# Kernel optimization log

Hardware: AMD Instinct MI355X
Metric: run time of the kernel (lower is better)

The kernel has to match this reference:

```python
import jax, jax.numpy as jnp
import numpy as np

NUM_POSES = 4096
NUM_PATCHES = 262144
NUM_OBS = 2097152


def setup_inputs() -> dict:
    key = jax.random.key(0)
    ks = jax.random.split(key, 7)
    poses = jax.random.normal(ks[0], (NUM_POSES, 7), dtype=jnp.float32)
    patch_coords = jax.random.normal(ks[1], (NUM_PATCHES, 2), dtype=jnp.float32)
    elevation_angle = jax.random.normal(ks[2], (NUM_PATCHES, 1), dtype=jnp.float32)
    poses_idx = jax.random.randint(ks[3], (NUM_OBS,), 0, NUM_POSES)
    patch_idx = jax.random.randint(ks[4], (NUM_OBS,), 0, NUM_PATCHES)
    target_coords = jax.random.normal(ks[5], (NUM_OBS, 3), dtype=jnp.float32)
    weights = jax.random.uniform(ks[6], (NUM_OBS, 1), dtype=jnp.float32)
    return {
        "poses": poses,
        "patch_coords": patch_coords,
        "elevation_angle": elevation_angle,
        "poses_idx": poses_idx,
        "patch_idx": patch_idx,
        "target_coords": target_coords,
        "weights": weights,
    }


def _se3_apply(pose7, pts):
    # pose7: [M,7] = (tx,ty,tz,qx,qy,qz,qw); pts: [M,3]
    # Equivalent to transform_matrix(pose) @ [pts; 1] (rotation by unit quaternion + translation)
    t = pose7[:, :3]
    q = pose7[:, 3:]
    q = q / jnp.linalg.norm(q, axis=-1, keepdims=True)  # pp.SE3 keeps unit quats
    qv, qw = q[:, :3], q[:, 3:4]
    uv = jnp.cross(qv, pts)                     # [M,3]
    rotated = pts + 2.0 * (qw * uv + jnp.cross(qv, uv))
    return rotated + t


def _cart2polar(xyz):
    # (x,y,z) -> (range, azimuth, elevation)
    x, y, z = xyz[:, 0], xyz[:, 1], xyz[:, 2]
    rho = jnp.sqrt(x * x + y * y)
    r = jnp.sqrt(rho * rho + z * z)
    az = jnp.arctan2(y, x)
    el = jnp.arctan2(z, rho)
    return jnp.stack([r, az, el], axis=1)


def reference(poses, patch_coords, elevation_angle, poses_idx, patch_idx, target_coords, weights):
    p = poses[poses_idx]                                            # [M,7] gather
    pts = jnp.concatenate(
        [patch_coords[patch_idx], elevation_angle[patch_idx]], axis=1
    )                                                               # [M,3] gather+cat
    proj = _cart2polar(_se3_apply(p, pts))                          # [M,3]
    residual = (proj - target_coords) * weights                     # [M,3]
    return residual
```

## Files before the change

kernel.cpp:

```cpp
#include <hip/hip_runtime.h>
#include <hip/hip_bf16.h>


#define NPOSES      4096
#define NPATCHES    262144
#define POSE_DWORDS (NPOSES * 7)
#define POSE_VEC4   (POSE_DWORDS / 4)

typedef float fvec4 __attribute__((ext_vector_type(4)));
typedef int   ivec4 __attribute__((ext_vector_type(4)));

__global__ __launch_bounds__(256) void pack_patches_kernel(
    const float* __restrict__ patch_coords, const float* __restrict__ elev,
    fvec4* __restrict__ patch4, int n)
{
    int i = blockIdx.x * blockDim.x + threadIdx.x;
    if (i >= n) return;
    float2 pc = *reinterpret_cast<const float2*>(patch_coords + (size_t)i * 2);
    patch4[i] = (fvec4){pc.x, pc.y, elev[i], 0.0f};
}

__global__ __launch_bounds__(1024) void ba_lds_kernel(
    const float* __restrict__ poses,
    const fvec4* __restrict__ patch4,
    const int*   __restrict__ poses_idx,
    const int*   __restrict__ patch_idx,
    const float* __restrict__ target,
    const float* __restrict__ weights,
    float*       __restrict__ out,
    int n4)
{
    extern __shared__ float lds[];
    int tid = threadIdx.x;

    {
        const fvec4* src = reinterpret_cast<const fvec4*>(poses);
        fvec4* dst = reinterpret_cast<fvec4*>(lds);
#pragma unroll
        for (int j = 0; j < POSE_VEC4 / 1024; ++j) {
            int idx = tid + j * 1024;
            dst[idx] = src[idx];
        }
    }
    __syncthreads();

    int i4 = blockIdx.x * blockDim.x + tid;
    if (i4 >= n4) return;

    ivec4 pidx = __builtin_nontemporal_load(reinterpret_cast<const ivec4*>(poses_idx) + i4);
    ivec4 qidx = __builtin_nontemporal_load(reinterpret_cast<const ivec4*>(patch_idx) + i4);
    fvec4 w4   = __builtin_nontemporal_load(reinterpret_cast<const fvec4*>(weights) + i4);
    const fvec4* tg4 = reinterpret_cast<const fvec4*>(target) + (size_t)i4 * 3;
    fvec4 t0 = __builtin_nontemporal_load(tg4 + 0);
    fvec4 t1 = __builtin_nontemporal_load(tg4 + 1);
    fvec4 t2 = __builtin_nontemporal_load(tg4 + 2);

    int   pi[4] = {pidx.x, pidx.y, pidx.z, pidx.w};
    int   qi[4] = {qidx.x, qidx.y, qidx.z, qidx.w};
    float ww[4] = {w4.x, w4.y, w4.z, w4.w};
    float tg[12] = {t0.x, t0.y, t0.z, t0.w,
                    t1.x, t1.y, t1.z, t1.w,
                    t2.x, t2.y, t2.z, t2.w};

    float res[12];

#pragma unroll
    for (int k = 0; k < 4; ++k) {
        const float* pl = lds + pi[k] * 7;
        float tx = pl[0], ty = pl[1], tz = pl[2];
        float qx = pl[3], qy = pl[4], qz = pl[5], qw = pl[6];
        float inv = rsqrtf(qx*qx + qy*qy + qz*qz + qw*qw);
        qx *= inv; qy *= inv; qz *= inv; qw *= inv;

        fvec4 pp = patch4[qi[k]];
        float px = pp.x, py = pp.y, pz = pp.z;

        float ux = qy*pz - qz*py;
        float uy = qz*px - qx*pz;
        float uz = qx*py - qy*px;
        float cx = qy*uz - qz*uy;
        float cy = qz*ux - qx*uz;
        float cz = qx*uy - qy*ux;
        float rx = px + 2.0f*(qw*ux + cx) + tx;
        float ry = py + 2.0f*(qw*uy + cy) + ty;
        float rz = pz + 2.0f*(qw*uz + cz) + tz;

        float rho = sqrtf(rx*rx + ry*ry);
        float r   = sqrtf(rho*rho + rz*rz);
        float az  = atan2f(ry, rx);
        float el  = atan2f(rz, rho);

        res[k*3 + 0] = (r  - tg[k*3 + 0]) * ww[k];
        res[k*3 + 1] = (az - tg[k*3 + 1]) * ww[k];
        res[k*3 + 2] = (el - tg[k*3 + 2]) * ww[k];
    }

    fvec4* o = reinterpret_cast<fvec4*>(out) + (size_t)i4 * 3;
    __builtin_nontemporal_store((fvec4){res[0], res[1], res[2],  res[3]},  o + 0);
    __builtin_nontemporal_store((fvec4){res[4], res[5], res[6],  res[7]},  o + 1);
    __builtin_nontemporal_store((fvec4){res[8], res[9], res[10], res[11]}, o + 2);
}

__global__ __launch_bounds__(256) void ba_fallback_kernel(
    const float* __restrict__ poses, const float* __restrict__ patch_coords,
    const float* __restrict__ elev, const int* __restrict__ poses_idx,
    const int* __restrict__ patch_idx, const float* __restrict__ target,
    const float* __restrict__ weights, float* __restrict__ out, int n)
{
    int i = blockIdx.x * blockDim.x + threadIdx.x;
    if (i >= n) return;
    int pi = poses_idx[i];
    int qi = patch_idx[i];
    const float* p = poses + (size_t)pi * 7;
    float tx = p[0], ty = p[1], tz = p[2];
    float qx = p[3], qy = p[4], qz = p[5], qw = p[6];
    float inv = rsqrtf(qx*qx + qy*qy + qz*qz + qw*qw);
    qx *= inv; qy *= inv; qz *= inv; qw *= inv;
    float2 pc = *reinterpret_cast<const float2*>(patch_coords + (size_t)qi * 2);
    float px = pc.x, py = pc.y, pz = elev[qi];
    float ux = qy*pz - qz*py, uy = qz*px - qx*pz, uz = qx*py - qy*px;
    float cx = qy*uz - qz*uy, cy = qz*ux - qx*uz, cz = qx*uy - qy*ux;
    float rx = px + 2.0f*(qw*ux + cx) + tx;
    float ry = py + 2.0f*(qw*uy + cy) + ty;
    float rz = pz + 2.0f*(qw*uz + cz) + tz;
    float rho = sqrtf(rx*rx + ry*ry);
    float r   = sqrtf(rho*rho + rz*rz);
    float az  = atan2f(ry, rx);
    float el  = atan2f(rz, rho);
    float w = weights[i];
    out[(size_t)i*3+0] = (r  - target[(size_t)i*3+0]) * w;
    out[(size_t)i*3+1] = (az - target[(size_t)i*3+1]) * w;
    out[(size_t)i*3+2] = (el - target[(size_t)i*3+2]) * w;
}

extern "C" void kernel_launch(void* const* d_in, const int* in_sizes, int n_in,
                              void* d_out, int out_size, void* d_ws, size_t ws_size,
                              hipStream_t stream) {
    const float* poses        = (const float*)d_in[0];
    const float* patch_coords = (const float*)d_in[1];
    const float* elev         = (const float*)d_in[2];
    const int*   poses_idx    = (const int*)d_in[3];
    const int*   patch_idx    = (const int*)d_in[4];
    const float* target       = (const float*)d_in[5];
    const float* weights      = (const float*)d_in[6];
    float*       out          = (float*)d_out;

    int n  = in_sizes[3];
    int n4 = n / 4;

    size_t patch_bytes = (size_t)NPATCHES * 16;
    size_t lds_bytes   = (size_t)POSE_DWORDS * 4;

    hipError_t attr_err = hipFuncSetAttribute(
        reinterpret_cast<const void*>(ba_lds_kernel),
        hipFuncAttributeMaxDynamicSharedMemorySize, (int)lds_bytes);

    if (attr_err == hipSuccess && ws_size >= patch_bytes) {
        fvec4* patch4 = (fvec4*)d_ws;
        pack_patches_kernel<<<(NPATCHES + 255) / 256, 256, 0, stream>>>(
            patch_coords, elev, patch4, NPATCHES);

        int block = 1024;
        int grid  = (n4 + block - 1) / block;
        ba_lds_kernel<<<grid, block, lds_bytes, stream>>>(
            poses, patch4, poses_idx, patch_idx, target, weights, out, n4);
    } else {
        ba_fallback_kernel<<<(n + 255) / 256, 256, 0, stream>>>(
            poses, patch_coords, elev, poses_idx, patch_idx, target, weights, out, n);
    }
}
```

Baseline: 45.76 us.

## Drop patch packing pre-pass and process eight observations per thread

Removes the separate kernel that packed patch coordinates and elevation into float4 workspace, and has the main kernel gather patch_coords (float2) and elev directly. Each thread now handles eight observations in two groups of four, halving the grid and amortizing the per-block LDS pose copy over more work. Nontemporal loads and stores are replaced with plain ones. The trade-off is two scattered gathers per observation instead of one, fewer threads in flight to hide gather latency, and lost cache-bypass hints on streaming traffic.

```diff
diff --git a/kernel.cpp b/kernel.cpp
--- a/kernel.cpp
+++ b/kernel.cpp
@@ -3,32 +3,22 @@
 
 
 #define NPOSES      4096
-#define NPATCHES    262144
 #define POSE_DWORDS (NPOSES * 7)
 #define POSE_VEC4   (POSE_DWORDS / 4)
 
 typedef float fvec4 __attribute__((ext_vector_type(4)));
 typedef int   ivec4 __attribute__((ext_vector_type(4)));
 
-__global__ __launch_bounds__(256) void pack_patches_kernel(
-    const float* __restrict__ patch_coords, const float* __restrict__ elev,
-    fvec4* __restrict__ patch4, int n)
-{
-    int i = blockIdx.x * blockDim.x + threadIdx.x;
-    if (i >= n) return;
-    float2 pc = *reinterpret_cast<const float2*>(patch_coords + (size_t)i * 2);
-    patch4[i] = (fvec4){pc.x, pc.y, elev[i], 0.0f};
-}
-
-__global__ __launch_bounds__(1024) void ba_lds_kernel(
+__global__ __launch_bounds__(1024) void ba_one_kernel(
     const float* __restrict__ poses,
-    const fvec4* __restrict__ patch4,
+    const float* __restrict__ patch_coords,
+    const float* __restrict__ elev,
     const int*   __restrict__ poses_idx,
     const int*   __restrict__ patch_idx,
     const float* __restrict__ target,
     const float* __restrict__ weights,
     float*       __restrict__ out,
-    int n4)
+    int n8)
 {
     extern __shared__ float lds[];
     int tid = threadIdx.x;
@@ -37,68 +27,73 @@
         const fvec4* src = reinterpret_cast<const fvec4*>(poses);
         fvec4* dst = reinterpret_cast<fvec4*>(lds);
 #pragma unroll
-        for (int j = 0; j < POSE_VEC4 / 1024; ++j) {
-            int idx = tid + j * 1024;
-            dst[idx] = src[idx];
-        }
+        for (int j = 0; j < POSE_VEC4 / 1024; ++j)
+            dst[tid + j * 1024] = src[tid + j * 1024];
     }
     __syncthreads();
 
-    int i4 = blockIdx.x * blockDim.x + tid;
-    if (i4 >= n4) return;
+    int i8 = blockIdx.x * blockDim.x + tid;
+    if (i8 >= n8) return;
 
-    ivec4 pidx = __builtin_nontemporal_load(reinterpret_cast<const ivec4*>(poses_idx) + i4);
-    ivec4 qidx = __builtin_nontemporal_load(reinterpret_cast<const ivec4*>(patch_idx) + i4);
-    fvec4 w4   = __builtin_nontemporal_load(reinterpret_cast<const fvec4*>(weights) + i4);
-    const fvec4* tg4 = reinterpret_cast<const fvec4*>(target) + (size_t)i4 * 3;
-    fvec4 t0 = __builtin_nontemporal_load(tg4 + 0);
-    fvec4 t1 = __builtin_nontemporal_load(tg4 + 1);
-    fvec4 t2 = __builtin_nontemporal_load(tg4 + 2);
-
-    int   pi[4] = {pidx.x, pidx.y, pidx.z, pidx.w};
-    int   qi[4] = {qidx.x, qidx.y, qidx.z, qidx.w};
-    float ww[4] = {w4.x, w4.y, w4.z, w4.w};
-    float tg[12] = {t0.x, t0.y, t0.z, t0.w,
-                    t1.x, t1.y, t1.z, t1.w,
-                    t2.x, t2.y, t2.z, t2.w};
-
-    float res[12];
+    const ivec4* pi4 = reinterpret_cast<const ivec4*>(poses_idx);
+    const ivec4* qi4 = reinterpret_cast<const ivec4*>(patch_idx);
+    const fvec4* w4p = reinterpret_cast<const fvec4*>(weights);
+    const fvec4* tg4 = reinterpret_cast<const fvec4*>(target) + (size_t)i8 * 6;
+    fvec4*       o4  = reinterpret_cast<fvec4*>(out) + (size_t)i8 * 6;
 
 #pragma unroll
-    for (int k = 0; k < 4; ++k) {
-        const float* pl = lds + pi[k] * 7;
-        float tx = pl[0], ty = pl[1], tz = pl[2];
-        float qx = pl[3], qy = pl[4], qz = pl[5], qw = pl[6];
-        float inv = rsqrtf(qx*qx + qy*qy + qz*qz + qw*qw);
-        qx *= inv; qy *= inv; qz *= inv; qw *= inv;
+    for (int g = 0; g < 2; ++g) {
+        ivec4 pidx = pi4[(size_t)i8 * 2 + g];
+        ivec4 qidx = qi4[(size_t)i8 * 2 + g];
+        fvec4 w4   = w4p[(size_t)i8 * 2 + g];
+        fvec4 t0 = tg4[g * 3 + 0];
+        fvec4 t1 = tg4[g * 3 + 1];
+        fvec4 t2 = tg4[g * 3 + 2];
 
-        fvec4 pp = patch4[qi[k]];
-        float px = pp.x, py = pp.y, pz = pp.z;
+        int   pi[4] = {pidx.x, pidx.y, pidx.z, pidx.w};
+        int   qi[4] = {qidx.x, qidx.y, qidx.z, qidx.w};
+        float ww[4] = {w4.x, w4.y, w4.z, w4.w};
+        float tg[12] = {t0.x, t0.y, t0.z, t0.w,
+                        t1.x, t1.y, t1.z, t1.w,
+                        t2.x, t2.y, t2.z, t2.w};
 
-        float ux = qy*pz - qz*py;
-        float uy = qz*px - qx*pz;
-        float uz = qx*py - qy*px;
-        float cx = qy*uz - qz*uy;
-        float cy = qz*ux - qx*uz;
-        float cz = qx*uy - qy*ux;
-        float rx = px + 2.0f*(qw*ux + cx) + tx;
-        float ry = py + 2.0f*(qw*uy + cy) + ty;
-        float rz = pz + 2.0f*(qw*uz + cz) + tz;
+        float res[12];
 
-        float rho = sqrtf(rx*rx + ry*ry);
-        float r   = sqrtf(rho*rho + rz*rz);
-        float az  = atan2f(ry, rx);
-        float el  = atan2f(rz, rho);
+#pragma unroll
+        for (int k = 0; k < 4; ++k) {
+            const float* pl = lds + pi[k] * 7;
+            float tx = pl[0], ty = pl[1], tz = pl[2];
+            float qx = pl[3], qy = pl[4], qz = pl[5], qw = pl[6];
+            float inv = rsqrtf(qx*qx + qy*qy + qz*qz + qw*qw);
+            qx *= inv; qy *= inv; qz *= inv; qw *= inv;
 
-        res[k*3 + 0] = (r  - tg[k*3 + 0]) * ww[k];
-        res[k*3 + 1] = (az - tg[k*3 + 1]) * ww[k];
-        res[k*3 + 2] = (el - tg[k*3 + 2]) * ww[k];
+            float2 pc = *reinterpret_cast<const float2*>(patch_coords + (size_t)qi[k] * 2);
+            float px = pc.x, py = pc.y, pz = elev[qi[k]];
+
+            float ux = qy*pz - qz*py;
+            float uy = qz*px - qx*pz;
+            float uz = qx*py - qy*px;
+            float cx = qy*uz - qz*uy;
+            float cy = qz*ux - qx*uz;
+            float cz = qx*uy - qy*ux;
+            float rx = px + 2.0f*(qw*ux + cx) + tx;
+            float ry = py + 2.0f*(qw*uy + cy) + ty;
+            float rz = pz + 2.0f*(qw*uz + cz) + tz;
+
+            float rho = sqrtf(rx*rx + ry*ry);
+            float r   = sqrtf(rho*rho + rz*rz);
+            float az  = atan2f(ry, rx);
+            float el  = atan2f(rz, rho);
+
+            res[k*3 + 0] = (r  - tg[k*3 + 0]) * ww[k];
+            res[k*3 + 1] = (az - tg[k*3 + 1]) * ww[k];
+            res[k*3 + 2] = (el - tg[k*3 + 2]) * ww[k];
+        }
+
+        o4[g * 3 + 0] = (fvec4){res[0], res[1], res[2],  res[3]};
+        o4[g * 3 + 1] = (fvec4){res[4], res[5], res[6],  res[7]};
+        o4[g * 3 + 2] = (fvec4){res[8], res[9], res[10], res[11]};
     }
-
-    fvec4* o = reinterpret_cast<fvec4*>(out) + (size_t)i4 * 3;
-    __builtin_nontemporal_store((fvec4){res[0], res[1], res[2],  res[3]},  o + 0);
-    __builtin_nontemporal_store((fvec4){res[4], res[5], res[6],  res[7]},  o + 1);
-    __builtin_nontemporal_store((fvec4){res[8], res[9], res[10], res[11]}, o + 2);
 }
 
 __global__ __launch_bounds__(256) void ba_fallback_kernel(
@@ -146,24 +141,20 @@
     float*       out          = (float*)d_out;
 
     int n  = in_sizes[3];
-    int n4 = n / 4;
+    int n8 = n / 8;
 
-    size_t patch_bytes = (size_t)NPATCHES * 16;
-    size_t lds_bytes   = (size_t)POSE_DWORDS * 4;
+    size_t lds_bytes = (size_t)POSE_DWORDS * 4;
 
     hipError_t attr_err = hipFuncSetAttribute(
-        reinterpret_cast<const void*>(ba_lds_kernel),
+        reinterpret_cast<const void*>(ba_one_kernel),
         hipFuncAttributeMaxDynamicSharedMemorySize, (int)lds_bytes);
 
-    if (attr_err == hipSuccess && ws_size >= patch_bytes) {
-        fvec4* patch4 = (fvec4*)d_ws;
-        pack_patches_kernel<<<(NPATCHES + 255) / 256, 256, 0, stream>>>(
-            patch_coords, elev, patch4, NPATCHES);
-
+    if (attr_err == hipSuccess) {
         int block = 1024;
-        int grid  = (n4 + block - 1) / block;
-        ba_lds_kernel<<<grid, block, lds_bytes, stream>>>(
-            poses, patch4, poses_idx, patch_idx, target, weights, out, n4);
+        int grid  = (n8 + block - 1) / block;
+        ba_one_kernel<<<grid, block, lds_bytes, stream>>>(
+            poses, patch_coords, elev, poses_idx, patch_idx,
+            target, weights, out, n8);
     } else {
         ba_fallback_kernel<<<(n + 255) / 256, 256, 0, stream>>>(
             poses, patch_coords, elev, poses_idx, patch_idx, target, weights, out, n);
```

Measured after the change: 50.12 us. 1.1x slower.
